# Kernel tuning notes

Hardware: AMD Instinct MI355X
Metric: run time of the kernel (lower is better)

## Reference

```python
import jax, jax.numpy as jnp
import numpy as np

B, S, DIN, DOUT = 4, 2048, 4096, 4096

def setup_inputs() -> dict:
    key = jax.random.key(0)
    k1, k2, k3 = jax.random.split(key, 3)
    x = jax.random.normal(k1, (B, S, DIN), dtype=jnp.float32)
    # kaiming-uniform-like scale for weight, uniform bias in [-1/sqrt(fan_in), 1/sqrt(fan_in)]
    bound_w = 1.0 / np.sqrt(DIN)
    weight = jax.random.uniform(k2, (DOUT, DIN), minval=-bound_w, maxval=bound_w, dtype=jnp.float32)
    bias = jax.random.uniform(k3, (DOUT,), minval=-bound_w, maxval=bound_w, dtype=jnp.float32)
    kk = jnp.asarray(1.0, dtype=jnp.float32)
    aa = jnp.asarray(1.0, dtype=jnp.float32)
    return {"x": x, "weight": weight, "bias": bias, "kk": kk, "aa": aa}

def reference(x, weight, bias, kk, aa):
    # Adiabatic binarization: soft-binarize weight with w_b = aa * tanh(kk * w),
    # then standard linear y = x @ w_b.T + bias. As kk -> inf, w_b -> aa*sign(w).
    w_b = aa * jnp.tanh(kk * weight)          # [DOUT, DIN]
    y = jnp.einsum('bsi,oi->bso', x, w_b)     # [B, S, DOUT]
    return y + bias
```

## Files before the change

kernel.cpp:

```cpp
#include <hip/hip_runtime.h>
#include <hip/hip_bf16.h>
#include <stdint.h>

#define B_DIM 4
#define S_DIM 2048
#define DIN   4096
#define DOUT  4096
#define M_TOT (B_DIM * S_DIM)

typedef __attribute__((ext_vector_type(8))) short  bf16x8;
typedef __attribute__((ext_vector_type(4))) float  f32x4;
typedef __attribute__((ext_vector_type(8))) unsigned short u16x8;
typedef __attribute__((ext_vector_type(4))) float  float4v;

__device__ __forceinline__ unsigned short f2b(float f) {
  union { float f; unsigned int i; } v; v.f = f;
  unsigned int r = v.i + 0x7FFFu + ((v.i >> 16) & 1u);
  return (unsigned short)(r >> 16);
}

__global__ void wb_tanh_kernel(const float4v* __restrict__ w, u16x8* __restrict__ wb,
                               const float* __restrict__ kk,
                               const float* __restrict__ aa, int n8) {
  const float k = kk[0];
  const float a = aa[0];
  int i = blockIdx.x * blockDim.x + threadIdx.x;
  const int stride = gridDim.x * blockDim.x;
  for (; i < n8; i += stride) {
    float4v v0 = w[2 * i];
    float4v v1 = w[2 * i + 1];
    u16x8 o;
#pragma unroll
    for (int j = 0; j < 4; ++j) o[j]     = f2b(a * tanhf(k * v0[j]));
#pragma unroll
    for (int j = 0; j < 4; ++j) o[j + 4] = f2b(a * tanhf(k * v1[j]));
    wb[i] = o;
  }
}

__global__ void x_cvt_kernel(const float4v* __restrict__ x, u16x8* __restrict__ xb, int n8) {
  int i = blockIdx.x * blockDim.x + threadIdx.x;
  const int stride = gridDim.x * blockDim.x;
  for (; i < n8; i += stride) {
    float4v v0 = x[2 * i];
    float4v v1 = x[2 * i + 1];
    u16x8 o;
#pragma unroll
    for (int j = 0; j < 4; ++j) o[j]     = f2b(v0[j]);
#pragma unroll
    for (int j = 0; j < 4; ++j) o[j + 4] = f2b(v1[j]);
    xb[i] = o;
  }
}

#define BM 128
#define BN 128
#define BK 32

__device__ __forceinline__ void glds16(const void* g, void* l) {
  __builtin_amdgcn_global_load_lds(
      (const __attribute__((address_space(1))) void*)g,
      (__attribute__((address_space(3))) void*)l,
      16, 0, 0);
}

__global__ __launch_bounds__(256, 3)
void gemm_bt_bias_kernel(const unsigned short* __restrict__ A,
                         const unsigned short* __restrict__ Bw,
                         const float* __restrict__ bias,
                         float* __restrict__ C) {
  __shared__ unsigned short As[BM * BK];
  __shared__ unsigned short Bs[BN * BK];

  const int tid  = threadIdx.x;
  const int wave = tid >> 6;
  const int lane = tid & 63;

  const int bm = blockIdx.y * BM;
  const int bn = blockIdx.x * BN;

  const int l4 = lane >> 2;
  const int lc = (lane & 3) * 8;
  const unsigned short* aG = A  + (size_t)(bm + wave * 32 + l4) * DIN + lc;
  const unsigned short* bG = Bw + (size_t)(bn + wave * 32 + l4) * DIN + lc;
  unsigned short* aL = &As[wave * 2 * 512];
  unsigned short* bL = &Bs[wave * 2 * 512];

  const int wm   = (wave >> 1) * 64;
  const int wn   = (wave & 1) * 64;
  const int quad = lane >> 4;
  const int r    = lane & 15;

  f32x4 acc[4][4] = {};

  for (int k0 = 0; k0 < DIN; k0 += BK) {
    glds16(aG,            aL);
    glds16(aG + 16 * DIN, aL + 512);
    glds16(bG,            bL);
    glds16(bG + 16 * DIN, bL + 512);
    aG += BK; bG += BK;
    __syncthreads();

    bf16x8 af[4], bfr[4];
#pragma unroll
    for (int mi = 0; mi < 4; ++mi)
      af[mi] = *(const bf16x8*)&As[(wm + mi * 16 + r) * BK + quad * 8];
#pragma unroll
    for (int ni = 0; ni < 4; ++ni)
      bfr[ni] = *(const bf16x8*)&Bs[(wn + ni * 16 + r) * BK + quad * 8];

#pragma unroll
    for (int mi = 0; mi < 4; ++mi)
#pragma unroll
      for (int ni = 0; ni < 4; ++ni)
        acc[mi][ni] = __builtin_amdgcn_mfma_f32_16x16x32_bf16(
            af[mi], bfr[ni], acc[mi][ni], 0, 0, 0);

    __syncthreads();
  }

#pragma unroll
  for (int ni = 0; ni < 4; ++ni) {
    const int col = bn + wn + ni * 16 + r;
    const float bv = bias[col];
#pragma unroll
    for (int mi = 0; mi < 4; ++mi) {
      const int row0 = bm + wm + mi * 16 + quad * 4;
#pragma unroll
      for (int e = 0; e < 4; ++e) {
        C[(size_t)(row0 + e) * DOUT + col] = acc[mi][ni][e] + bv;
      }
    }
  }
}

extern "C" void kernel_launch(void* const* d_in, const int* in_sizes, int n_in,
                              void* d_out, int out_size, void* d_ws, size_t ws_size,
                              hipStream_t stream) {
  const float* x    = (const float*)d_in[0];
  const float* w    = (const float*)d_in[1];
  const float* bias = (const float*)d_in[2];
  const float* kk   = (const float*)d_in[3];
  const float* aa   = (const float*)d_in[4];
  float* out = (float*)d_out;

  unsigned short* wb = (unsigned short*)d_ws;
  unsigned short* xb = wb + (size_t)DOUT * DIN;

  wb_tanh_kernel<<<2048, 256, 0, stream>>>(
      (const float4v*)w, (u16x8*)wb, kk, aa, DOUT * DIN / 8);
  x_cvt_kernel<<<4096, 256, 0, stream>>>(
      (const float4v*)x, (u16x8*)xb, M_TOT * DIN / 8);

  dim3 grid(DOUT / BN, M_TOT / BM);
  gemm_bt_bias_kernel<<<grid, 256, 0, stream>>>(xb, wb, bias, out);
}
```

Before: 566.6 us.

## Rewrite GEMM as 256x256 tile, 8-wave, double-buffered pipelined kernel with LDS swizzle

Replaces the 128x128x32 GEMM with a 256x256x64 tile kernel using 512 threads, double-buffered LDS filled by global_load_lds, and an XOR swizzle to avoid bank conflicts. Loads for upcoming k-tiles are interleaved with MFMA phases using explicit barriers, waitcnt and setprio, and block indices are remapped for L2 locality. The aim is higher arithmetic intensity and hiding load latency behind MFMA. In exchange it uses more registers and LDS per block, which lowers occupancy, and the hand-placed synchronization is fragile.

```diff
diff --git a/kernel.cpp b/kernel.cpp
--- a/kernel.cpp
+++ b/kernel.cpp
@@ -1,5 +1,4 @@
 #include <hip/hip_runtime.h>
-#include <hip/hip_bf16.h>
 #include <stdint.h>
 
 #define B_DIM 4
@@ -53,83 +52,143 @@
   }
 }
 
-#define BM 128
-#define BN 128
-#define BK 32
-
-__device__ __forceinline__ void glds16(const void* g, void* l) {
+#define BM 256
+#define BN 256
+#define BK 64
+#define NT (DIN / BK)
+
+__device__ __forceinline__ void glds16(const unsigned short* g, unsigned short* l) {
   __builtin_amdgcn_global_load_lds(
       (const __attribute__((address_space(1))) void*)g,
       (__attribute__((address_space(3))) void*)l,
       16, 0, 0);
 }
 
-__global__ __launch_bounds__(256, 3)
-void gemm_bt_bias_kernel(const unsigned short* __restrict__ A,
-                         const unsigned short* __restrict__ Bw,
-                         const float* __restrict__ bias,
-                         float* __restrict__ C) {
-  __shared__ unsigned short As[BM * BK];
-  __shared__ unsigned short Bs[BN * BK];
+#define BARX()    __builtin_amdgcn_s_barrier()
+#define LGKM0()   asm volatile("s_waitcnt lgkmcnt(0)" ::: "memory")
+#define WAITVM4() asm volatile("s_waitcnt vmcnt(4)" ::: "memory")
+#define WAITVM0() asm volatile("s_waitcnt vmcnt(0)" ::: "memory")
+
+#define RD_A(dst, mi, BUFB)                                                   \
+  dst[0] = *(const bf16x8*)(aRd + (BUFB) + (mi) * 2048 + blk0);               \
+  dst[1] = *(const bf16x8*)(aRd + (BUFB) + (mi) * 2048 + blk1);
+
+#define RD_B(ni, BUFB)                                                        \
+  bfr[ni][0] = *(const bf16x8*)(bRd + (BUFB) + (ni) * 2048 + blk0);           \
+  bfr[ni][1] = *(const bf16x8*)(bRd + (BUFB) + (ni) * 2048 + blk1);
+
+#define MFMA_PH(AF, MB)                                                       \
+  __builtin_amdgcn_s_setprio(1);                                              \
+  {                                                                           \
+    _Pragma("unroll")                                                         \
+    for (int ks = 0; ks < 2; ++ks)                                            \
+      _Pragma("unroll")                                                       \
+      for (int i = 0; i < 2; ++i)                                             \
+        _Pragma("unroll")                                                     \
+        for (int ni = 0; ni < 4; ++ni)                                        \
+          acc[(MB) + i][ni] = __builtin_amdgcn_mfma_f32_16x16x32_bf16(        \
+              AF[i][ks], bfr[ni][ks], acc[(MB) + i][ni], 0, 0, 0);            \
+  }                                                                           \
+  __builtin_amdgcn_s_setprio(0);
+
+#define KTILE(t, BUFB)                                                        \
+  {                                                                           \
+                                  \
+    RD_B(0, BUFB); RD_B(1, BUFB); RD_B(2, BUFB); RD_B(3, BUFB);               \
+    RD_A(afA[0], 0, BUFB); RD_A(afA[1], 1, BUFB);                             \
+    issue_half(((t) + 1) * 4 + 2); issue_half(((t) + 1) * 4 + 3);             \
+    BARX(); LGKM0();                                                          \
+    MFMA_PH(afA, 0);                                                          \
+    BARX();                                                                   \
+                           \
+    RD_A(afB[0], 2, BUFB); RD_A(afB[1], 3, BUFB);                             \
+    RD_A(afA[0], 4, BUFB); RD_A(afA[1], 5, BUFB);                             \
+    BARX(); LGKM0();                                                          \
+    MFMA_PH(afB, 2);                                                          \
+    BARX();                                                                   \
+                                      \
+    RD_A(afB[0], 6, BUFB); RD_A(afB[1], 7, BUFB);                             \
+    BARX(); LGKM0();                                                          \
+    MFMA_PH(afA, 4);                                                          \
+    BARX();                                                                   \
+       \
+    issue_half(((t) + 2) * 4 + 0); issue_half(((t) + 2) * 4 + 1);             \
+    BARX(); LGKM0();                                                          \
+    MFMA_PH(afB, 6);                                                          \
+    if ((t) + 2 < NT) { WAITVM4(); } else { WAITVM0(); }                      \
+    BARX();                                                                   \
+  }
+
+__global__ __launch_bounds__(512, 2)
+void gemm256_kernel(const unsigned short* __restrict__ A,
+                    const unsigned short* __restrict__ Bw,
+                    const float* __restrict__ bias,
+                    float* __restrict__ C) {
+  __shared__ unsigned short lds[2][2][BM * BK];
 
   const int tid  = threadIdx.x;
-  const int wave = tid >> 6;
+  const int wv   = tid >> 6;
   const int lane = tid & 63;
-
-  const int bm = blockIdx.y * BM;
-  const int bn = blockIdx.x * BN;
-
-  const int l4 = lane >> 2;
-  const int lc = (lane & 3) * 8;
-  const unsigned short* aG = A  + (size_t)(bm + wave * 32 + l4) * DIN + lc;
-  const unsigned short* bG = Bw + (size_t)(bn + wave * 32 + l4) * DIN + lc;
-  unsigned short* aL = &As[wave * 2 * 512];
-  unsigned short* bL = &Bs[wave * 2 * 512];
-
-  const int wm   = (wave >> 1) * 64;
-  const int wn   = (wave & 1) * 64;
+  const int l15  = lane & 15;
   const int quad = lane >> 4;
-  const int r    = lane & 15;
-
-  f32x4 acc[4][4] = {};
-
-  for (int k0 = 0; k0 < DIN; k0 += BK) {
-    glds16(aG,            aL);
-    glds16(aG + 16 * DIN, aL + 512);
-    glds16(bG,            bL);
-    glds16(bG + 16 * DIN, bL + 512);
-    aG += BK; bG += BK;
-    __syncthreads();
-
-    bf16x8 af[4], bfr[4];
-#pragma unroll
-    for (int mi = 0; mi < 4; ++mi)
-      af[mi] = *(const bf16x8*)&As[(wm + mi * 16 + r) * BK + quad * 8];
-#pragma unroll
-    for (int ni = 0; ni < 4; ++ni)
-      bfr[ni] = *(const bf16x8*)&Bs[(wn + ni * 16 + r) * BK + quad * 8];
-
-#pragma unroll
-    for (int mi = 0; mi < 4; ++mi)
-#pragma unroll
-      for (int ni = 0; ni < 4; ++ni)
-        acc[mi][ni] = __builtin_amdgcn_mfma_f32_16x16x32_bf16(
-            af[mi], bfr[ni], acc[mi][ni], 0, 0, 0);
-
-    __syncthreads();
-  }
-
+  const int l7   = lane & 7;
+  const int rlan = lane >> 3;
+
+  const int swz = ((blockIdx.x & 7) << 6) | (blockIdx.x >> 3);
+  const int bm  = (swz & 31) << 8;
+  const int bn  = (swz >> 5) << 8;
+
+  const unsigned short* aLane = A  + (size_t)(bm + wv * 16 + rlan) * DIN + ((l7 ^ rlan) << 3);
+  const unsigned short* bLane = Bw + (size_t)(bn + wv * 16 + rlan) * DIN + ((l7 ^ rlan) << 3);
+
+  auto issue_half = [&](int idx) {
+    const int kt = idx >> 2;
+    if (kt >= NT) return;
+    const int hh  = idx & 3;
+    const int mat = hh >> 1;
+    const int hr  = hh & 1;
+    const unsigned short* g =
+        (mat ? bLane : aLane) + (size_t)hr * (128 * DIN) + (size_t)kt * BK;
+    unsigned short* l = &lds[kt & 1][mat][hr * (128 * BK) + wv * (16 * BK)];
+    glds16(g, l);
+    glds16(g + 8 * DIN, l + 8 * BK);
+  };
+
+  issue_half(0); issue_half(1); issue_half(2); issue_half(3);
+  issue_half(4); issue_half(5);
+
+  const int hA   = wv >> 2;
+  const int hB   = (wv & 3) >> 1;
+  const int wloc = wv & 1;
+  const char* aRd = (const char*)&lds[0][0][0] + hA * 16384 + l15 * 128;
+  const char* bRd = (const char*)&lds[0][1][0] + hB * 16384 + wloc * 8192 + l15 * 128;
+  const int blk0 = ((0 + quad) ^ l7) * 16;
+  const int blk1 = ((4 + quad) ^ l7) * 16;
+
+  f32x4  acc[8][4] = {};
+  bf16x8 bfr[4][2], afA[2][2], afB[2][2];
+
+  WAITVM4();
+  BARX();
+
+#pragma unroll 1
+  for (int t = 0; t < NT; t += 2) {
+    KTILE(t, 0);
+    KTILE(t + 1, 65536);
+  }
+
+  const int wm = (wv >> 2) * 128;
+  const int wn = (wv & 3) * 64;
 #pragma unroll
   for (int ni = 0; ni < 4; ++ni) {
-    const int col = bn + wn + ni * 16 + r;
+    const int col = bn + wn + ni * 16 + l15;
     const float bv = bias[col];
 #pragma unroll
-    for (int mi = 0; mi < 4; ++mi) {
+    for (int mi = 0; mi < 8; ++mi) {
       const int row0 = bm + wm + mi * 16 + quad * 4;
 #pragma unroll
-      for (int e = 0; e < 4; ++e) {
+      for (int e = 0; e < 4; ++e)
         C[(size_t)(row0 + e) * DOUT + col] = acc[mi][ni][e] + bv;
-      }
     }
   }
 }
@@ -152,6 +211,5 @@
   x_cvt_kernel<<<4096, 256, 0, stream>>>(
       (const float4v*)x, (u16x8*)xb, M_TOT * DIN / 8);
 
-  dim3 grid(DOUT / BN, M_TOT / BM);
-  gemm_bt_bias_kernel<<<grid, 256, 0, stream>>>(xb, wb, bias, out);
-}
+  gemm256_kernel<<<dim3(512), dim3(512), 0, stream>>>(xb, wb, bias, out);
+}
```

After: 532.5 us. -6.0%, faster.
